# Optimization experiments

Hardware: AMD Instinct MI355X
Metric: run time of the kernel (lower is better)

## Reference

```python
import jax, jax.numpy as jnp
import numpy as np
import math

B, N, C = 4, 2048, 768
H = 12
DFF = 4 * C
EPS = 1e-5

def _layernorm(x, gamma, beta):
    mu = jnp.mean(x, axis=-1, keepdims=True)
    var = jnp.var(x, axis=-1, keepdims=True)
    return (x - mu) * jax.lax.rsqrt(var + EPS) * gamma + beta

def setup_inputs() -> dict:
    key = jax.random.key(0)
    ks = jax.random.split(key, 12)
    s = 0.02
    return {
        "x": jax.random.normal(ks[0], (B, N, C), jnp.float32),
        "Wqkv": jax.random.normal(ks[1], (C, 3 * C), jnp.float32) * s,
        "bqkv": jnp.zeros((3 * C,), jnp.float32),
        "Wproj": jax.random.normal(ks[2], (C, C), jnp.float32) * s,
        "bproj": jnp.zeros((C,), jnp.float32),
        "g1": jnp.ones((C,), jnp.float32),
        "b1": jnp.zeros((C,), jnp.float32),
        "g2": jnp.ones((C,), jnp.float32),
        "b2": jnp.zeros((C,), jnp.float32),
        "Wfc1": jax.random.normal(ks[3], (C, DFF), jnp.float32) * s,
        "bfc1": jnp.zeros((DFF,), jnp.float32),
        "Wfc2": jax.random.normal(ks[4], (DFF, C), jnp.float32) * s,
        "bfc2": jnp.zeros((C,), jnp.float32),
    }

def reference(x, Wqkv, bqkv, Wproj, bproj, g1, b1, g2, b2, Wfc1, bfc1, Wfc2, bfc2):
    head_dim = C // H
    qkv = x @ Wqkv + bqkv                      # [B,N,3C]
    q, k, v = jnp.split(qkv, 3, axis=-1)
    # [B,N,C] -> [B,H,N,hd]
    def to_heads(t):
        return t.reshape(B, N, H, head_dim).transpose(0, 2, 1, 3)
    q, k, v = to_heads(q), to_heads(k), to_heads(v)
    attn = jnp.einsum('bhqd,bhkd->bhqk', q, k) / math.sqrt(head_dim)
    attn = jax.nn.softmax(attn, axis=-1)       # dropout p=0 -> identity
    out = jnp.einsum('bhqk,bhkd->bhqd', attn, v)
    out = out.transpose(0, 2, 1, 3).reshape(B, N, C)
    out = out @ Wproj + bproj
    x = _layernorm(x + out, g1, b1)
    h = jax.nn.gelu(x @ Wfc1 + bfc1, approximate=False) @ Wfc2 + bfc2
    x = _layernorm(x + h, g2, b2)
    return x
```

## Files before the change

### kernel.cpp

```cpp
#include <hip/hip_runtime.h>

typedef __bf16 bf16;
typedef __bf16 bf16x2 __attribute__((ext_vector_type(2)));
typedef __bf16 bf16x4 __attribute__((ext_vector_type(4)));
typedef __bf16 bf16x8 __attribute__((ext_vector_type(8)));
typedef float  f32x4  __attribute__((ext_vector_type(4)));
typedef float  f32x16 __attribute__((ext_vector_type(16)));
typedef int    intx4  __attribute__((ext_vector_type(4)));

#define BB 4
#define SEQ 2048
#define CH 768
#define NH 12
#define HD 64
#define DFF 3072
#define MROWS (BB * SEQ)
#define C3 (3 * CH)
#define NBH (BB * NH)

__device__ inline f32x16 mfma32(bf16x8 a, bf16x8 b, f32x16 c) {
    return __builtin_amdgcn_mfma_f32_32x32x16_bf16(a, b, c, 0, 0, 0);
}
__device__ inline f32x4 mfma16(bf16x8 a, bf16x8 b, f32x4 c) {
    return __builtin_amdgcn_mfma_f32_16x16x32_bf16(a, b, c, 0, 0, 0);
}
__device__ inline void gload16(const void* g, void* l) {
    __builtin_amdgcn_global_load_lds((const __attribute__((address_space(1))) void*)g,
                                     (__attribute__((address_space(3))) void*)l, 16, 0, 0);
}
__device__ inline void plswap_i(int& x, int& y) {
    asm volatile("v_permlane32_swap_b32 %0, %1" : "+v"(x), "+v"(y));
}
__device__ inline void plswap_f(float& x, float& y) {
    asm volatile("v_permlane32_swap_b32 %0, %1" : "+v"(x), "+v"(y));
}
__device__ inline int bcast_lo(int v) { int x = v, y = v; plswap_i(x, y); return y; }
__device__ inline int bcast_hi(int v) { int x = v, y = v; plswap_i(x, y); return x; }

__global__ __launch_bounds__(256) void prep_kernel(
    const float* __restrict__ x, bf16* __restrict__ xb,
    const float* __restrict__ Wqkv, bf16* __restrict__ WqkvT,
    const float* __restrict__ Wproj, bf16* __restrict__ WprojT,
    const float* __restrict__ Wfc1, bf16* __restrict__ Wfc1T,
    const float* __restrict__ Wfc2, bf16* __restrict__ Wfc2T) {
    __shared__ bf16 t[32][33];
    int bid = blockIdx.x;
    if (bid < 6144) {
        int i = (bid * 256 + threadIdx.x) * 4;
        f32x4 v = *(const f32x4*)&x[i];
        bf16x4 o;
        #pragma unroll
        for (int j = 0; j < 4; ++j) o[j] = (bf16)v[j];
        *(bf16x4*)&xb[i] = o;
        return;
    }
    bid -= 6144;
    const float* src;
    bf16* dst;
    int R, Cc, wT;
    if (bid < 1728)      { src = Wqkv;  dst = WqkvT;  R = CH;  Cc = C3;  wT = 72; }
    else if (bid < 2304) { bid -= 1728; src = Wproj; dst = WprojT; R = CH;  Cc = CH;  wT = 24; }
    else if (bid < 4608) { bid -= 2304; src = Wfc1;  dst = Wfc1T;  R = CH;  Cc = DFF; wT = 96; }
    else                 { bid -= 4608; src = Wfc2;  dst = Wfc2T;  R = DFF; Cc = CH;  wT = 24; }
    int tx = threadIdx.x & 31, ty = threadIdx.x >> 5;
    int c0 = (bid % wT) * 32, r0 = (bid / wT) * 32;
    #pragma unroll
    for (int i = 0; i < 32; i += 8)
        t[ty + i][tx] = (bf16)src[(size_t)(r0 + ty + i) * Cc + c0 + tx];
    __syncthreads();
    #pragma unroll
    for (int i = 0; i < 32; i += 8)
        dst[(size_t)(c0 + ty + i) * R + r0 + tx] = t[tx][ty + i];
}

__global__ void transpose_v(const bf16* __restrict__ qkvb, bf16* __restrict__ vt) {
    __shared__ bf16 t[32][33];
    int tx = threadIdx.x & 31, ty = threadIdx.x >> 5;
    int n0 = blockIdx.x * 32, d0 = blockIdx.y * 32, bh = blockIdx.z;
    int b = bh / NH, h = bh - b * NH;
    #pragma unroll
    for (int i = 0; i < 32; i += 8)
        t[ty + i][tx] = qkvb[((size_t)b * SEQ + n0 + ty + i) * C3 + 2 * CH + h * HD + d0 + tx];
    __syncthreads();
    #pragma unroll
    for (int i = 0; i < 32; i += 8)
        vt[((size_t)bh * HD + d0 + ty + i) * SEQ + n0 + tx] = t[tx][ty + i];
}

template <int OMODE>
__global__ __launch_bounds__(256) void gemm_bt(const bf16* __restrict__ A,
                                               const bf16* __restrict__ Bt,
                                               const float* __restrict__ bias,
                                               void* __restrict__ Cout,
                                               int M, int N, int K, int lda) {
    __shared__ __align__(16) bf16 As[2][128][32];
    __shared__ __align__(16) bf16 Bs[2][128][32];
    const int nwg = gridDim.x * gridDim.y;
    const int orig = blockIdx.y * gridDim.x + blockIdx.x;
    const int wg = (orig & 7) * (nwg >> 3) + (orig >> 3);
    const int bm = (wg / gridDim.x) * 128, bn = (wg % gridDim.x) * 128;
    const int kbeg = blockIdx.z * K;
    const int tid = threadIdx.x;
    const int lane = tid & 63, w = tid >> 6;
    const int wr = w >> 1, wc = w & 1;
    const int lr = lane & 15, lg = lane >> 4;

    const int srow = tid >> 2, schk = (tid & 3) * 8;
    const bf16* gA0 = A + (size_t)(bm + srow) * lda + kbeg + schk;
    const bf16* gA1 = A + (size_t)(bm + 64 + srow) * lda + kbeg + schk;
    const bf16* gB0 = Bt + (size_t)(bn + srow) * lda + kbeg + schk;
    const bf16* gB1 = Bt + (size_t)(bn + 64 + srow) * lda + kbeg + schk;

    auto stage = [&](int buf, int kofs) {
        gload16(gA0 + kofs, &As[buf][srow][schk]);
        gload16(gA1 + kofs, &As[buf][64 + srow][schk]);
        gload16(gB0 + kofs, &Bs[buf][srow][schk]);
        gload16(gB1 + kofs, &Bs[buf][64 + srow][schk]);
    };

    f32x4 acc[4][4];
    #pragma unroll
    for (int i = 0; i < 4; ++i)
        #pragma unroll
        for (int j = 0; j < 4; ++j) acc[i][j] = (f32x4){0.f, 0.f, 0.f, 0.f};

    stage(0, 0);
    int cur = 0;
    for (int k0 = 0; k0 < K; k0 += 32) {
        __syncthreads();
        if (k0 + 32 < K) stage(cur ^ 1, k0 + 32);
        bf16x8 af[4], bfr[4];
        #pragma unroll
        for (int mi = 0; mi < 4; ++mi)
            af[mi] = *(const bf16x8*)&As[cur][wr * 64 + mi * 16 + lr][lg * 8];
        #pragma unroll
        for (int ni = 0; ni < 4; ++ni)
            bfr[ni] = *(const bf16x8*)&Bs[cur][wc * 64 + ni * 16 + lr][lg * 8];
        #pragma unroll
        for (int mi = 0; mi < 4; ++mi)
            #pragma unroll
            for (int ni = 0; ni < 4; ++ni)
                acc[mi][ni] = mfma16(af[mi], bfr[ni], acc[mi][ni]);
        cur ^= 1;
    }

    #pragma unroll
    for (int mi = 0; mi < 4; ++mi) {
        #pragma unroll
        for (int ni = 0; ni < 4; ++ni) {
            int col = bn + wc * 64 + ni * 16 + lr;
            float bsv = (OMODE == 3) ? 0.f : bias[col];
            #pragma unroll
            for (int r = 0; r < 4; ++r) {
                int row = bm + wr * 64 + mi * 16 + lg * 4 + r;
                float v = acc[mi][ni][r] + bsv;
                if (OMODE == 2) v = 0.5f * v * (1.0f + erff(v * 0.70710678118654752f));
                if (OMODE == 0)
                    ((float*)Cout)[(size_t)row * N + col] = v;
                else if (OMODE == 3)
                    ((bf16*)Cout)[(size_t)blockIdx.z * M * N + (size_t)row * N + col] = (bf16)v;
                else
                    ((bf16*)Cout)[(size_t)row * N + col] = (bf16)v;
            }
        }
    }
}

#define C2F 0.18033688011112f
#define THR2 11.5416f
__global__ __launch_bounds__(256, 3) void attn_kernel(const bf16* __restrict__ qkvb,
                                                      const bf16* __restrict__ vt,
                                                      bf16* __restrict__ outb) {
    __shared__ __align__(16) bf16 Kl[2][64 * 64];
    __shared__ __align__(16) bf16 Vl[2][64 * 64];
    const int tid = threadIdx.x;
    const int w = tid >> 6, lane = tid & 63;
    const int lq = lane & 31;
    const int hi = lane >> 5;
    const int lin = blockIdx.x;
    const int xcd = lin & 7, slot = lin >> 3;
    const int bh = xcd * 6 + (slot >> 4);
    const int qt = slot & 15;
    const int b = bh / NH, h = bh - b * NH;
    const int q0 = qt * 128 + w * 32;

    const bf16* qbase = qkvb + (size_t)b * SEQ * C3 + h * HD;
    const bf16* kbase = qbase + CH;
    const bf16* vbase = vt + (size_t)bh * HD * SEQ;

    const int srow = tid >> 3;
    const int ksc = (tid & 7) ^ (srow & 7);
    const bf16* gk0 = kbase + (size_t)srow * C3 + ksc * 8;
    const bf16* gk1 = kbase + (size_t)(srow + 32) * C3 + ksc * 8;
    const bf16* gv0 = vbase + (size_t)srow * SEQ + ksc * 8;
    const bf16* gv1 = vbase + (size_t)(srow + 32) * SEQ + ksc * 8;
    const int ldst = tid * 8;

    bf16x8 qf[4];
    #pragma unroll
    for (int ks = 0; ks < 4; ++ks)
        qf[ks] = *(const bf16x8*)&qbase[(size_t)(q0 + lq) * C3 + ks * 16 + hi * 8];

    f32x16 o0 = {0.f}, o1 = {0.f};
    float m = -3.0e38f, l = 0.f;

    const int swz = lq & 7;

    auto stage = [&](int buf, int kv0) {
        gload16(gk0 + (size_t)kv0 * C3, &Kl[buf][ldst]);
        gload16(gk1 + (size_t)kv0 * C3, &Kl[buf][2048 + ldst]);
        gload16(gv0 + kv0, &Vl[buf][ldst]);
        gload16(gv1 + kv0, &Vl[buf][2048 + ldst]);
    };

    auto process = [&](const bf16* Kb, const bf16* Vb) {
        f32x16 st0 = {0.f}, st1 = {0.f};
        #pragma unroll
        for (int ks = 0; ks < 4; ++ks) {
            int c = 8 * ((2 * ks + hi) ^ swz);
            bf16x8 k0 = *(const bf16x8*)&Kb[lq * 64 + c];
            bf16x8 k1 = *(const bf16x8*)&Kb[(32 + lq) * 64 + c];
            st0 = mfma32(k0, qf[ks], st0);
            st1 = mfma32(k1, qf[ks], st1);
        }
        float t_[8];
        #pragma unroll
        for (int r = 0; r < 8; ++r)
            t_[r] = fmaxf(fmaxf(st0[r], st0[r + 8]), fmaxf(st1[r], st1[r + 8]));
        #pragma unroll
        for (int r = 0; r < 4; ++r) t_[r] = fmaxf(t_[r], t_[r + 4]);
        float lmax = fmaxf(fmaxf(t_[0], t_[1]), fmaxf(t_[2], t_[3]));
        float mxa = lmax, mxb = lmax;
        plswap_f(mxa, mxb);
        float m2x = fmaxf(mxa, mxb) * C2F;
        if (!__all(m2x <= m + THR2)) {
            float mn = fmaxf(m, m2x);
            float alpha = __builtin_amdgcn_exp2f(m - mn);
            m = mn;
            l *= alpha;
            #pragma unroll
            for (int r = 0; r < 16; ++r) {
                int qr = (r & 3) + 8 * (r >> 2) + 4 * hi;
                float ar = __shfl(alpha, qr);
                o0[r] *= ar;
                o1[r] *= ar;
            }
        }
        bf16x8 pa[4];
        float ps0, ps1;
        {
            float p[16];
            #pragma unroll
            for (int r = 0; r < 16; ++r) p[r] = __builtin_amdgcn_exp2f(fmaf(st0[r], C2F, -m));
            float s0[8];
            #pragma unroll
            for (int r = 0; r < 8; ++r) s0[r] = p[r] + p[r + 8];
            #pragma unroll
            for (int r = 0; r < 4; ++r) s0[r] += s0[r + 4];
            ps0 = (s0[0] + s0[1]) + (s0[2] + s0[3]);
            int a[8];
            #pragma unroll
            for (int i = 0; i < 8; ++i) {
                bf16x2 t2 = {(bf16)p[2 * i], (bf16)p[2 * i + 1]};
                a[i] = __builtin_bit_cast(int, t2);
            }
            intx4 f0 = {bcast_lo(a[0]), bcast_lo(a[1]), bcast_hi(a[2]), bcast_hi(a[3])};
            intx4 f1 = {bcast_lo(a[4]), bcast_lo(a[5]), bcast_hi(a[6]), bcast_hi(a[7])};
            pa[0] = __builtin_bit_cast(bf16x8, f0);
            pa[1] = __builtin_bit_cast(bf16x8, f1);
        }
        {
            float p[16];
            #pragma unroll
            for (int r = 0; r < 16; ++r) p[r] = __builtin_amdgcn_exp2f(fmaf(st1[r], C2F, -m));
            float s0[8];
            #pragma unroll
            for (int r = 0; r < 8; ++r) s0[r] = p[r] + p[r + 8];
            #pragma unroll
            for (int r = 0; r < 4; ++r) s0[r] += s0[r + 4];
            ps1 = (s0[0] + s0[1]) + (s0[2] + s0[3]);
            int a[8];
            #pragma unroll
            for (int i = 0; i < 8; ++i) {
                bf16x2 t2 = {(bf16)p[2 * i], (bf16)p[2 * i + 1]};
                a[i] = __builtin_bit_cast(int, t2);
            }
            intx4 f0 = {bcast_lo(a[0]), bcast_lo(a[1]), bcast_hi(a[2]), bcast_hi(a[3])};
            intx4 f1 = {bcast_lo(a[4]), bcast_lo(a[5]), bcast_hi(a[6]), bcast_hi(a[7])};
            pa[2] = __builtin_bit_cast(bf16x8, f0);
            pa[3] = __builtin_bit_cast(bf16x8, f1);
        }
        float ps = ps0 + ps1;
        float pA = ps, pB = ps;
        plswap_f(pA, pB);
        l += pA + pB;
        #pragma unroll
        for (int c = 0; c < 4; ++c) {
            int cc = 8 * ((2 * c + hi) ^ swz);
            bf16x8 v0 = *(const bf16x8*)&Vb[lq * 64 + cc];
            bf16x8 v1 = *(const bf16x8*)&Vb[(32 + lq) * 64 + cc];
            o0 = mfma32(pa[c], v0, o0);
            o1 = mfma32(pa[c], v1, o1);
        }
    };

    stage(0, 0);
    __syncthreads();
    for (int t = 0; t < 32; t += 2) {
        stage(1, (t + 1) * 64);
        process(Kl[0], Vl[0]);
        __syncthreads();
        stage(0, (t + 2 < 32 ? t + 2 : 31) * 64);
        process(Kl[1], Vl[1]);
        __syncthreads();
    }

    float linv = 1.0f / l;
    const size_t obase = (size_t)b * SEQ * CH + h * HD;
    #pragma unroll
    for (int r = 0; r < 16; ++r) {
        int qr = (r & 3) + 8 * (r >> 2) + 4 * hi;
        float lr_ = __shfl(linv, qr);
        size_t rowo = obase + (size_t)(q0 + qr) * CH;
        outb[rowo + lq] = (bf16)(o0[r] * lr_);
        outb[rowo + 32 + lq] = (bf16)(o1[r] * lr_);
    }
}

template <int XBF16, int OUTF32, int NP>
__global__ __launch_bounds__(256) void add_ln(const void* __restrict__ xin,
                                              const bf16* __restrict__ tp,
                                              const float* __restrict__ bias,
                                              const float* __restrict__ g,
                                              const float* __restrict__ bt,
                                              void* __restrict__ yout) {
    const int row = blockIdx.x;
    const size_t base = (size_t)row * CH;
    const int tid = threadIdx.x;
    float v[3];
    #pragma unroll
    for (int k = 0; k < 3; ++k) {
        int c = tid + k * 256;
        float xv = XBF16 ? (float)((const bf16*)xin)[base + c]
                         : ((const float*)xin)[base + c];
        float acc = xv + bias[c];
        #pragma unroll
        for (int z = 0; z < NP; ++z)
            acc += (float)tp[(size_t)z * MROWS * CH + base + c];
        v[k] = acc;
    }
    __shared__ float red[4];
    float s = v[0] + v[1] + v[2];
    #pragma unroll
    for (int off = 32; off >= 1; off >>= 1) s += __shfl_down(s, off);
    if ((tid & 63) == 0) red[tid >> 6] = s;
    __syncthreads();
    float mean = (red[0] + red[1] + red[2] + red[3]) * (1.0f / 768.0f);
    float q = 0.f;
    #pragma unroll
    for (int k = 0; k < 3; ++k) {
        float d = v[k] - mean;
        q += d * d;
    }
    __syncthreads();
    #pragma unroll
    for (int off = 32; off >= 1; off >>= 1) q += __shfl_down(q, off);
    if ((tid & 63) == 0) red[tid >> 6] = q;
    __syncthreads();
    float var = (red[0] + red[1] + red[2] + red[3]) * (1.0f / 768.0f);
    float rstd = rsqrtf(var + 1e-5f);
    #pragma unroll
    for (int k = 0; k < 3; ++k) {
        int c = tid + k * 256;
        float out = (v[k] - mean) * rstd * g[c] + bt[c];
        if (OUTF32) ((float*)yout)[base + c] = out;
        else        ((bf16*)yout)[base + c] = (bf16)out;
    }
}

extern "C" void kernel_launch(void* const* d_in, const int* in_sizes, int n_in,
                              void* d_out, int out_size, void* d_ws, size_t ws_size,
                              hipStream_t stream) {
    const float* x    = (const float*)d_in[0];
    const float* Wqkv = (const float*)d_in[1];
    const float* bqkv = (const float*)d_in[2];
    const float* Wproj= (const float*)d_in[3];
    const float* bproj= (const float*)d_in[4];
    const float* g1   = (const float*)d_in[5];
    const float* b1   = (const float*)d_in[6];
    const float* g2   = (const float*)d_in[7];
    const float* b2   = (const float*)d_in[8];
    const float* Wfc1 = (const float*)d_in[9];
    const float* bfc1 = (const float*)d_in[10];
    const float* Wfc2 = (const float*)d_in[11];
    const float* bfc2 = (const float*)d_in[12];

    char* ws = (char*)d_ws;
    size_t off = 0;
    auto alloc = [&](size_t bytes) -> void* {
        void* p = ws + off;
        off += (bytes + 255) & ~(size_t)255;
        return p;
    };

    bf16* xb     = (bf16*)alloc((size_t)MROWS * CH * 2);
    bf16* WqkvT  = (bf16*)alloc((size_t)C3 * CH * 2);
    bf16* WprojT = (bf16*)alloc((size_t)CH * CH * 2);
    bf16* Wfc1T  = (bf16*)alloc((size_t)DFF * CH * 2);
    bf16* Wfc2T  = (bf16*)alloc((size_t)CH * DFF * 2);
    bf16* qkvb   = (bf16*)alloc((size_t)MROWS * C3 * 2);
    bf16* vtb    = (bf16*)alloc((size_t)NBH * HD * SEQ * 2);
    bf16* attnb  = (bf16*)alloc((size_t)MROWS * CH * 2);
    bf16* tmpP   = (bf16*)alloc((size_t)2 * MROWS * CH * 2);
    bf16* y1b    = (bf16*)alloc((size_t)MROWS * CH * 2);
    bf16* hb     = (bf16*)alloc((size_t)MROWS * DFF * 2);

    prep_kernel<<<13056, 256, 0, stream>>>(x, xb, Wqkv, WqkvT, Wproj, WprojT,
                                           Wfc1, Wfc1T, Wfc2, Wfc2T);
    gemm_bt<1><<<dim3(C3 / 128, MROWS / 128), 256, 0, stream>>>(xb, WqkvT, bqkv, qkvb, MROWS, C3, CH, CH);
    transpose_v<<<dim3(SEQ / 32, HD / 32, NBH), 256, 0, stream>>>(qkvb, vtb);
    attn_kernel<<<768, 256, 0, stream>>>(qkvb, vtb, attnb);
    gemm_bt<3><<<dim3(CH / 128, MROWS / 128, 2), 256, 0, stream>>>(attnb, WprojT, nullptr, tmpP, MROWS, CH, CH / 2, CH);
    add_ln<0, 0, 2><<<MROWS, 256, 0, stream>>>(x, tmpP, bproj, g1, b1, y1b);
    gemm_bt<2><<<dim3(DFF / 128, MROWS / 128), 256, 0, stream>>>(y1b, Wfc1T, bfc1, hb, MROWS, DFF, CH, CH);
    gemm_bt<3><<<dim3(CH / 128, MROWS / 128, 2), 256, 0, stream>>>(hb, Wfc2T, nullptr, tmpP, MROWS, CH, DFF / 2, DFF);
    add_ln<1, 1, 2><<<MROWS, 256, 0, stream>>>(y1b, tmpP, bfc2, g2, b2, (float*)d_out);
}
```

Baseline: 294.6 us.

## Fuse head-split and V transpose into QKV GEMM epilogue; use tanh GELU

The QKV GEMM epilogue now writes Q and K in per-head [bh,seq,hd] layout and V pre-transposed as [bh,hd,seq]. This removes the separate transpose_v kernel and lets attention load K rows contiguously. The FC1 epilogue also replaces the erf GELU with a tanh approximation computed through exp2, which costs less per element but departs slightly from the exact GELU. V stores in the GEMM epilogue are strided along seq, which may be uncoalesced.

Measured after the change: 313.1 us. 6.3% more time.

```diff
diff --git a/kernel.cpp b/kernel.cpp
--- a/kernel.cpp
+++ b/kernel.cpp
@@ -17,6 +17,7 @@
 #define MROWS (BB * SEQ)
 #define C3 (3 * CH)
 #define NBH (BB * NH)
+#define QKOFF ((size_t)NBH * SEQ * HD)
 
 __device__ inline f32x16 mfma32(bf16x8 a, bf16x8 b, f32x16 c) {
     return __builtin_amdgcn_mfma_f32_32x32x16_bf16(a, b, c, 0, 0, 0);
@@ -71,20 +72,6 @@
     #pragma unroll
     for (int i = 0; i < 32; i += 8)
         dst[(size_t)(c0 + ty + i) * R + r0 + tx] = t[tx][ty + i];
-}
-
-__global__ void transpose_v(const bf16* __restrict__ qkvb, bf16* __restrict__ vt) {
-    __shared__ bf16 t[32][33];
-    int tx = threadIdx.x & 31, ty = threadIdx.x >> 5;
-    int n0 = blockIdx.x * 32, d0 = blockIdx.y * 32, bh = blockIdx.z;
-    int b = bh / NH, h = bh - b * NH;
-    #pragma unroll
-    for (int i = 0; i < 32; i += 8)
-        t[ty + i][tx] = qkvb[((size_t)b * SEQ + n0 + ty + i) * C3 + 2 * CH + h * HD + d0 + tx];
-    __syncthreads();
-    #pragma unroll
-    for (int i = 0; i < 32; i += 8)
-        vt[((size_t)bh * HD + d0 + ty + i) * SEQ + n0 + tx] = t[tx][ty + i];
 }
 
 template <int OMODE>
@@ -154,13 +141,31 @@
             for (int r = 0; r < 4; ++r) {
                 int row = bm + wr * 64 + mi * 16 + lg * 4 + r;
                 float v = acc[mi][ni][r] + bsv;
-                if (OMODE == 2) v = 0.5f * v * (1.0f + erff(v * 0.70710678118654752f));
-                if (OMODE == 0)
+                if (OMODE == 2) {
+                    float z = fmaf(0.044715f * v * v, v, v) * 1.5957691216f;
+                    float e = __builtin_amdgcn_exp2f(z * 1.4426950409f);
+                    v = v * (e / (e + 1.0f));
+                }
+                if (OMODE == 0) {
                     ((float*)Cout)[(size_t)row * N + col] = v;
-                else if (OMODE == 3)
+                } else if (OMODE == 3) {
                     ((bf16*)Cout)[(size_t)blockIdx.z * M * N + (size_t)row * N + col] = (bf16)v;
-                else
+                } else if (OMODE == 4) {
+                    bf16* base = (bf16*)Cout;
+                    int sect = col / CH;
+                    int rem  = col - sect * CH;
+                    int h = rem >> 6, d = rem & 63;
+                    int bb = row >> 11, s = row & 2047;
+                    int bh = bb * NH + h;
+                    if (sect == 0)
+                        base[((size_t)bh * SEQ + s) * HD + d] = (bf16)v;
+                    else if (sect == 1)
+                        base[QKOFF + ((size_t)bh * SEQ + s) * HD + d] = (bf16)v;
+                    else
+                        base[2 * QKOFF + ((size_t)bh * HD + d) * SEQ + s] = (bf16)v;
+                } else {
                     ((bf16*)Cout)[(size_t)row * N + col] = (bf16)v;
+                }
             }
         }
     }
@@ -168,8 +173,7 @@
 
 #define C2F 0.18033688011112f
 #define THR2 11.5416f
-__global__ __launch_bounds__(256, 3) void attn_kernel(const bf16* __restrict__ qkvb,
-                                                      const bf16* __restrict__ vt,
+__global__ __launch_bounds__(256, 3) void attn_kernel(const bf16* __restrict__ qkv3,
                                                       bf16* __restrict__ outb) {
     __shared__ __align__(16) bf16 Kl[2][64 * 64];
     __shared__ __align__(16) bf16 Vl[2][64 * 64];
@@ -184,14 +188,14 @@
     const int b = bh / NH, h = bh - b * NH;
     const int q0 = qt * 128 + w * 32;
 
-    const bf16* qbase = qkvb + (size_t)b * SEQ * C3 + h * HD;
-    const bf16* kbase = qbase + CH;
-    const bf16* vbase = vt + (size_t)bh * HD * SEQ;
+    const bf16* qd = qkv3 + (size_t)bh * SEQ * HD;
+    const bf16* kd = qkv3 + QKOFF + (size_t)bh * SEQ * HD;
+    const bf16* vbase = qkv3 + 2 * QKOFF + (size_t)bh * HD * SEQ;
 
     const int srow = tid >> 3;
     const int ksc = (tid & 7) ^ (srow & 7);
-    const bf16* gk0 = kbase + (size_t)srow * C3 + ksc * 8;
-    const bf16* gk1 = kbase + (size_t)(srow + 32) * C3 + ksc * 8;
+    const bf16* gk0 = kd + (size_t)srow * HD + ksc * 8;
+    const bf16* gk1 = kd + (size_t)(srow + 32) * HD + ksc * 8;
     const bf16* gv0 = vbase + (size_t)srow * SEQ + ksc * 8;
     const bf16* gv1 = vbase + (size_t)(srow + 32) * SEQ + ksc * 8;
     const int ldst = tid * 8;
@@ -199,7 +203,7 @@
     bf16x8 qf[4];
     #pragma unroll
     for (int ks = 0; ks < 4; ++ks)
-        qf[ks] = *(const bf16x8*)&qbase[(size_t)(q0 + lq) * C3 + ks * 16 + hi * 8];
+        qf[ks] = *(const bf16x8*)&qd[(size_t)(q0 + lq) * HD + ks * 16 + hi * 8];
 
     f32x16 o0 = {0.f}, o1 = {0.f};
     float m = -3.0e38f, l = 0.f;
@@ -207,8 +211,8 @@
     const int swz = lq & 7;
 
     auto stage = [&](int buf, int kv0) {
-        gload16(gk0 + (size_t)kv0 * C3, &Kl[buf][ldst]);
-        gload16(gk1 + (size_t)kv0 * C3, &Kl[buf][2048 + ldst]);
+        gload16(gk0 + (size_t)kv0 * HD, &Kl[buf][ldst]);
+        gload16(gk1 + (size_t)kv0 * HD, &Kl[buf][2048 + ldst]);
         gload16(gv0 + kv0, &Vl[buf][ldst]);
         gload16(gv1 + kv0, &Vl[buf][2048 + ldst]);
     };
@@ -408,8 +412,7 @@
     bf16* WprojT = (bf16*)alloc((size_t)CH * CH * 2);
     bf16* Wfc1T  = (bf16*)alloc((size_t)DFF * CH * 2);
     bf16* Wfc2T  = (bf16*)alloc((size_t)CH * DFF * 2);
-    bf16* qkvb   = (bf16*)alloc((size_t)MROWS * C3 * 2);
-    bf16* vtb    = (bf16*)alloc((size_t)NBH * HD * SEQ * 2);
+    bf16* qkv3   = (bf16*)alloc((size_t)3 * QKOFF * 2);
     bf16* attnb  = (bf16*)alloc((size_t)MROWS * CH * 2);
     bf16* tmpP   = (bf16*)alloc((size_t)2 * MROWS * CH * 2);
     bf16* y1b    = (bf16*)alloc((size_t)MROWS * CH * 2);
@@ -417,9 +420,8 @@
 
     prep_kernel<<<13056, 256, 0, stream>>>(x, xb, Wqkv, WqkvT, Wproj, WprojT,
                                            Wfc1, Wfc1T, Wfc2, Wfc2T);
-    gemm_bt<1><<<dim3(C3 / 128, MROWS / 128), 256, 0, stream>>>(xb, WqkvT, bqkv, qkvb, MROWS, C3, CH, CH);
-    transpose_v<<<dim3(SEQ / 32, HD / 32, NBH), 256, 0, stream>>>(qkvb, vtb);
-    attn_kernel<<<768, 256, 0, stream>>>(qkvb, vtb, attnb);
+    gemm_bt<4><<<dim3(C3 / 128, MROWS / 128), 256, 0, stream>>>(xb, WqkvT, bqkv, qkv3, MROWS, C3, CH, CH);
+    attn_kernel<<<768, 256, 0, stream>>>(qkv3, attnb);
     gemm_bt<3><<<dim3(CH / 128, MROWS / 128, 2), 256, 0, stream>>>(attnb, WprojT, nullptr, tmpP, MROWS, CH, CH / 2, CH);
     add_ln<0, 0, 2><<<MROWS, 256, 0, stream>>>(x, tmpP, bproj, g1, b1, y1b);
     gemm_bt<2><<<dim3(DFF / 128, MROWS / 128), 256, 0, stream>>>(y1b, Wfc1T, bfc1, hb, MROWS, DFF, CH, CH);
```
